# Optimization experiments

Hardware: AMD Instinct MI355X
Metric: run time of the kernel (lower is better)

Reference implementation:

```python
import jax, jax.numpy as jnp
import numpy as np
from jax import lax

T, H, I, E = 1024, 2048, 1024, 16
G, TOPK_GROUP, TOP_K = 4, 2, 4
ROUTED_SCALE = 2.5
W_SCALE = 0.02  # keep activations in a sane range


def setup_inputs() -> dict:
    key = jax.random.key(0)
    ks = jax.random.split(key, 7)
    return {
        "hidden_states": jax.random.normal(ks[0], (T, H), jnp.float32),
        "gate_w": jax.random.normal(ks[1], (E, H), jnp.float32) * W_SCALE,
        "e_bias": jax.random.normal(ks[2], (E,), jnp.float32),
        "w_gate_up": jax.random.normal(ks[3], (E, 2 * I, H), jnp.float32) * W_SCALE,
        "w_down": jax.random.normal(ks[4], (E, H, I), jnp.float32) * W_SCALE,
        "shared_w_gate_up": jax.random.normal(ks[5], (2 * I, H), jnp.float32) * W_SCALE,
        "shared_w_down": jax.random.normal(ks[6], (H, I), jnp.float32) * W_SCALE,
    }


def _grouped_topk(scores, e_bias):
    # scores: sigmoid router scores [T, E]
    scores_b = scores + e_bias[None, :]
    # group score = sum of top-2 biased scores within each group (bias branch)
    group_scores = jnp.sum(lax.top_k(scores_b.reshape(-1, G, E // G), 2)[0], axis=-1)  # [T, G]
    _, group_idx = lax.top_k(group_scores, TOPK_GROUP)  # [T, topk_group]
    group_mask = jnp.any(jax.nn.one_hot(group_idx, G, dtype=jnp.bool_), axis=1)  # [T, G]
    score_mask = jnp.repeat(group_mask, E // G, axis=-1)  # [T, E]
    tmp = jnp.where(score_mask, scores_b, 0.0)
    _, topk_ids = lax.top_k(tmp, TOP_K)  # [T, K]
    topk_w = jnp.take_along_axis(scores, topk_ids, axis=1)  # weights from UNbiased scores
    topk_w = topk_w / jnp.sum(topk_w, axis=-1, keepdims=True)  # renormalize
    return topk_w, topk_ids


def _silu_and_mul(gu):
    g, u = jnp.split(gu, 2, axis=-1)
    return jax.nn.silu(g) * u


def reference(hidden_states, gate_w, e_bias, w_gate_up, w_down,
              shared_w_gate_up, shared_w_down):
    x = hidden_states  # [T, H]
    # shared expert MLP
    shared = _silu_and_mul(x @ shared_w_gate_up.T) @ shared_w_down.T  # [T, H]
    # router
    logits = x @ gate_w.T                      # [T, E]
    scores = jax.nn.sigmoid(logits)
    topk_w, topk_ids = _grouped_topk(scores, e_bias)
    # dense combine weights [T, E] (zero for unselected experts)
    combine = jnp.zeros((T, E), x.dtype).at[jnp.arange(T)[:, None], topk_ids].add(topk_w)
    # routed experts: SwiGLU per expert, combined with routing weights
    gu = jnp.einsum('th,eih->tei', x, w_gate_up)        # [T, E, 2I]
    a = _silu_and_mul(gu)                               # [T, E, I]
    routed = jnp.einsum('tei,ehi,te->th', a, w_down, combine)  # [T, H]
    return routed * ROUTED_SCALE + shared
```

## Files before the change

kernel.cpp:

```cpp
#include <hip/hip_runtime.h>
#include <math.h>

typedef __bf16 bf16;
typedef bf16 bf16x4 __attribute__((ext_vector_type(4)));
typedef bf16 bf16x8 __attribute__((ext_vector_type(8)));
typedef float f32x4 __attribute__((ext_vector_type(4)));

#define T_TOK   1024
#define H_DIM   2048
#define I_DIM   1024
#define E_NUM   16
#define NPAIR_R 4096
#define NPAIR   5120

typedef __attribute__((address_space(3))) unsigned int lds_uint;
typedef __attribute__((address_space(1))) const unsigned int gbl_uint;
__device__ __forceinline__ void gld16(const void* g, void* l) {
  __builtin_amdgcn_global_load_lds((gbl_uint*)g, (lds_uint*)l, 16, 0, 0);
}

__global__ __launch_bounds__(256) void router_kernel(
    const float* __restrict__ x, const float* __restrict__ gate_w,
    const float* __restrict__ e_bias, bf16* __restrict__ xb,
    int* __restrict__ topk_ids, float* __restrict__ topk_w,
    int* __restrict__ counts)
{
  int t = blockIdx.x;
  int tid = threadIdx.x;
  float acc[16];
#pragma unroll
  for (int e = 0; e < 16; ++e) acc[e] = 0.f;
  const float* xr = x + (size_t)t * H_DIM;
  bf16* xbr = xb + (size_t)t * H_DIM;
  for (int h = tid; h < H_DIM; h += 256) {
    float xv = xr[h];
    xbr[h] = (bf16)xv;
#pragma unroll
    for (int e = 0; e < 16; ++e) acc[e] += xv * gate_w[e * H_DIM + h];
  }
#pragma unroll
  for (int e = 0; e < 16; ++e) {
#pragma unroll
    for (int off = 32; off >= 1; off >>= 1)
      acc[e] += __shfl_down(acc[e], off, 64);
  }
  __shared__ float red[4][16];
  int lane = tid & 63, wave = tid >> 6;
  if (lane == 0) {
#pragma unroll
    for (int e = 0; e < 16; ++e) red[wave][e] = acc[e];
  }
  __syncthreads();
  if (tid == 0) {
    float scores[16], sb[16];
    for (int e = 0; e < 16; ++e) {
      float l = red[0][e] + red[1][e] + red[2][e] + red[3][e];
      float s = 1.f / (1.f + expf(-l));
      scores[e] = s;
      sb[e] = s + e_bias[e];
    }
    float gs[4];
    for (int g = 0; g < 4; ++g) {
      float b1 = -1e30f, b2 = -1e30f;
      for (int j = 0; j < 4; ++j) {
        float v = sb[g * 4 + j];
        if (v > b1) { b2 = b1; b1 = v; }
        else if (v > b2) b2 = v;
      }
      gs[g] = b1 + b2;
    }
    int g1 = 0; float bv = gs[0];
    for (int g = 1; g < 4; ++g) if (gs[g] > bv) { bv = gs[g]; g1 = g; }
    int g2 = -1; float bv2 = -1e30f;
    for (int g = 0; g < 4; ++g) if (g != g1 && gs[g] > bv2) { bv2 = gs[g]; g2 = g; }
    float tmp[16];
    for (int e = 0; e < 16; ++e) {
      int grp = e >> 2;
      tmp[e] = (grp == g1 || grp == g2) ? sb[e] : 0.0f;
    }
    bool used[16] = {false};
    int ids[4]; float wv[4]; float wsum = 0.f;
    for (int k = 0; k < 4; ++k) {
      int bi = 0; float bvv = -1e30f;
      for (int i = 0; i < 16; ++i)
        if (!used[i] && tmp[i] > bvv) { bvv = tmp[i]; bi = i; }
      used[bi] = true;
      ids[k] = bi; wv[k] = scores[bi]; wsum += scores[bi];
    }
    float inv = 1.f / wsum;
    for (int k = 0; k < 4; ++k) {
      topk_ids[t * 4 + k] = ids[k];
      topk_w[t * 4 + k] = wv[k] * inv;
      atomicAdd(&counts[ids[k]], 1);
    }
  }
}

__global__ void offsets_kernel(const int* __restrict__ counts, int* __restrict__ off)
{
  if (threadIdx.x == 0 && blockIdx.x == 0) {
    int s = 0;
    for (int e = 0; e < 16; ++e) { off[e] = s; s += counts[e]; }
    off[16] = s;
  }
}

__global__ __launch_bounds__(256) void scatter_kernel(
    const int* __restrict__ topk_ids, const float* __restrict__ topk_w,
    const int* __restrict__ off, int* __restrict__ cursor,
    int* __restrict__ pair_token, float* __restrict__ pair_scale)
{
  int i = blockIdx.x * 256 + threadIdx.x;
  if (i < NPAIR_R) {
    int e = topk_ids[i];
    float w = topk_w[i];
    int pos = atomicAdd(&cursor[e], 1);
    int idx = off[e] + pos;
    pair_token[idx] = i >> 2;
    pair_scale[idx] = 2.5f * w;
  } else if (i < NPAIR) {
    pair_token[i] = i - NPAIR_R;
    pair_scale[i] = 1.0f;
  }
}

__global__ __launch_bounds__(256, 3) void gateup_kernel(
    const bf16* __restrict__ xb, const float* __restrict__ w_gu,
    const float* __restrict__ s_wgu,
    const int* __restrict__ off, const int* __restrict__ pair_token,
    bf16* __restrict__ a_buf)
{
  const int nt = blockIdx.x;
  const int mt = blockIdx.y;
  const int e  = blockIdx.z;
  const int poff = (e < 16) ? off[e]     : NPAIR_R;
  const int pend = (e < 16) ? off[e + 1] : NPAIR;
  const int cnt  = pend - poff;
  if (mt * 128 >= cnt) return;
  const float* __restrict__ B = (e < 16) ? (w_gu + (size_t)e * 2 * I_DIM * H_DIM) : s_wgu;

  __shared__ __align__(16) bf16  As[2][128 * 32];
  __shared__ __align__(16) float Bs[2][128 * 32];

  const int tid = threadIdx.x;
  const int lane = tid & 63;
  const int wave = tid >> 6;
  const int wm = wave >> 1, wn = wave & 1;
  const int c0 = lane >> 4;
  const int fr = lane & 15;

  const bf16* aptr[2];
#pragma unroll
  for (int s = 0; s < 2; ++s) {
    int idx = s * 256 + tid;
    int ar = idx >> 2, ach = idx & 3;
    int sch = ach ^ ((ar >> 1) & 3);
    int p = poff + mt * 128 + ar;
    aptr[s] = xb + (size_t)pair_token[p] * H_DIM + sch * 8;
  }
  const float* bptr[4];
#pragma unroll
  for (int s = 0; s < 4; ++s) {
    int idx = s * 256 + tid;
    int br = idx >> 3, bch = idx & 7;
    int sch = bch ^ (br & 7);
    int rg = nt * 64 + br + (br >= 64 ? 960 : 0);
    bptr[s] = B + (size_t)rg * H_DIM + sch * 4;
  }
  int a_off[4];
#pragma unroll
  for (int mi = 0; mi < 4; ++mi) {
    int ar = wm * 64 + mi * 16 + fr;
    a_off[mi] = ar * 64 + ((c0 ^ ((ar >> 1) & 3)) << 4);
  }
  int b_off[4];
#pragma unroll
  for (int ni = 0; ni < 4; ++ni) {
    int br = wn * 32 + (ni & 1) * 16 + fr + (ni >> 1) * 64;
    b_off[ni] = br * 128 + (((2 * c0) ^ (br & 7)) << 4);
  }

  f32x4 acc[4][4];
  f32x4 zz = {0.f, 0.f, 0.f, 0.f};
#pragma unroll
  for (int mi = 0; mi < 4; ++mi)
#pragma unroll
    for (int ni = 0; ni < 4; ++ni) acc[mi][ni] = zz;

  const int ldso = tid * 16;
#pragma unroll
  for (int s = 0; s < 2; ++s)
    gld16(aptr[s], (char*)(&As[0][0]) + s * 4096 + ldso);
#pragma unroll
  for (int s = 0; s < 4; ++s)
    gld16(bptr[s], (char*)(&Bs[0][0]) + s * 4096 + ldso);
  __syncthreads();

  int cur = 0;
  const int NT = H_DIM / 32;
  for (int t = 0; t < NT; ++t) {
    if (t + 1 < NT) {
      const int k0 = (t + 1) * 32;
#pragma unroll
      for (int s = 0; s < 2; ++s)
        gld16(aptr[s] + k0, (char*)(&As[cur ^ 1][0]) + s * 4096 + ldso);
#pragma unroll
      for (int s = 0; s < 4; ++s)
        gld16(bptr[s] + k0, (char*)(&Bs[cur ^ 1][0]) + s * 4096 + ldso);
    }
    const char* Ab = (const char*)(&As[cur][0]);
    const char* Bb = (const char*)(&Bs[cur][0]);
    bf16x8 af[4], bv[4];
#pragma unroll
    for (int mi = 0; mi < 4; ++mi)
      af[mi] = *(const bf16x8*)(Ab + a_off[mi]);
#pragma unroll
    for (int ni = 0; ni < 4; ++ni) {
      f32x4 x0 = *(const f32x4*)(Bb + b_off[ni]);
      f32x4 x1 = *(const f32x4*)(Bb + (b_off[ni] ^ 16));
      bf16x8 b;
      b[0] = (bf16)x0[0]; b[1] = (bf16)x0[1]; b[2] = (bf16)x0[2]; b[3] = (bf16)x0[3];
      b[4] = (bf16)x1[0]; b[5] = (bf16)x1[1]; b[6] = (bf16)x1[2]; b[7] = (bf16)x1[3];
      bv[ni] = b;
    }
#pragma unroll
    for (int mi = 0; mi < 4; ++mi)
#pragma unroll
      for (int ni = 0; ni < 4; ++ni)
        acc[mi][ni] = __builtin_amdgcn_mfma_f32_16x16x32_bf16(af[mi], bv[ni], acc[mi][ni], 0, 0, 0);
    __syncthreads();
    cur ^= 1;
  }

#pragma unroll
  for (int mi = 0; mi < 4; ++mi) {
#pragma unroll
    for (int reg = 0; reg < 4; ++reg) {
      int r = wm * 64 + mi * 16 + c0 * 4 + reg;
      int rl = mt * 128 + r;
      if (rl < cnt) {
        size_t p = (size_t)(poff + rl);
        bf16* orow = a_buf + p * I_DIM + nt * 64 + wn * 32 + fr;
#pragma unroll
        for (int ni = 0; ni < 2; ++ni) {
          float g = acc[mi][ni][reg];
          float u = acc[mi][ni + 2][reg];
          float sg = g / (1.f + expf(-g));
          orow[ni * 16] = (bf16)(sg * u);
        }
      }
    }
  }
}

__global__ __launch_bounds__(256, 3) void down_kernel(
    const bf16* __restrict__ a_buf, const float* __restrict__ w_dn,
    const float* __restrict__ s_wdn,
    const int* __restrict__ off, const int* __restrict__ pair_token,
    const float* __restrict__ pair_scale, float* __restrict__ out)
{
  const int nt = blockIdx.x;
  const int mt = blockIdx.y;
  const int e  = blockIdx.z;
  const int poff = (e < 16) ? off[e]     : NPAIR_R;
  const int pend = (e < 16) ? off[e + 1] : NPAIR;
  const int cnt  = pend - poff;
  if (mt * 128 >= cnt) return;
  const float* __restrict__ B = (e < 16) ? (w_dn + (size_t)e * H_DIM * I_DIM) : s_wdn;

  __shared__ __align__(16) bf16  As[2][128 * 32];
  __shared__ __align__(16) float Bs[2][128 * 32];

  const int tid = threadIdx.x;
  const int lane = tid & 63;
  const int wave = tid >> 6;
  const int wm = wave >> 1, wn = wave & 1;
  const int c0 = lane >> 4;
  const int fr = lane & 15;

  const bf16* aptr[2];
#pragma unroll
  for (int s = 0; s < 2; ++s) {
    int idx = s * 256 + tid;
    int ar = idx >> 2, ach = idx & 3;
    int sch = ach ^ ((ar >> 1) & 3);
    int p = poff + mt * 128 + ar;
    aptr[s] = a_buf + (size_t)p * I_DIM + sch * 8;
  }
  const float* bptr[4];
#pragma unroll
  for (int s = 0; s < 4; ++s) {
    int idx = s * 256 + tid;
    int br = idx >> 3, bch = idx & 7;
    int sch = bch ^ (br & 7);
    bptr[s] = B + (size_t)(nt * 128 + br) * I_DIM + sch * 4;
  }
  int a_off[4];
#pragma unroll
  for (int mi = 0; mi < 4; ++mi) {
    int ar = wm * 64 + mi * 16 + fr;
    a_off[mi] = ar * 64 + ((c0 ^ ((ar >> 1) & 3)) << 4);
  }
  int b_off[4];
#pragma unroll
  for (int ni = 0; ni < 4; ++ni) {
    int br = wn * 64 + ni * 16 + fr;
    b_off[ni] = br * 128 + (((2 * c0) ^ (br & 7)) << 4);
  }

  f32x4 acc[4][4];
  f32x4 zz = {0.f, 0.f, 0.f, 0.f};
#pragma unroll
  for (int mi = 0; mi < 4; ++mi)
#pragma unroll
    for (int ni = 0; ni < 4; ++ni) acc[mi][ni] = zz;

  const int ldso = tid * 16;
#pragma unroll
  for (int s = 0; s < 2; ++s)
    gld16(aptr[s], (char*)(&As[0][0]) + s * 4096 + ldso);
#pragma unroll
  for (int s = 0; s < 4; ++s)
    gld16(bptr[s], (char*)(&Bs[0][0]) + s * 4096 + ldso);
  __syncthreads();

  int cur = 0;
  const int NT = I_DIM / 32;
  for (int t = 0; t < NT; ++t) {
    if (t + 1 < NT) {
      const int k0 = (t + 1) * 32;
#pragma unroll
      for (int s = 0; s < 2; ++s)
        gld16(aptr[s] + k0, (char*)(&As[cur ^ 1][0]) + s * 4096 + ldso);
#pragma unroll
      for (int s = 0; s < 4; ++s)
        gld16(bptr[s] + k0, (char*)(&Bs[cur ^ 1][0]) + s * 4096 + ldso);
    }
    const char* Ab = (const char*)(&As[cur][0]);
    const char* Bb = (const char*)(&Bs[cur][0]);
    bf16x8 af[4], bv[4];
#pragma unroll
    for (int mi = 0; mi < 4; ++mi)
      af[mi] = *(const bf16x8*)(Ab + a_off[mi]);
#pragma unroll
    for (int ni = 0; ni < 4; ++ni) {
      f32x4 x0 = *(const f32x4*)(Bb + b_off[ni]);
      f32x4 x1 = *(const f32x4*)(Bb + (b_off[ni] ^ 16));
      bf16x8 b;
      b[0] = (bf16)x0[0]; b[1] = (bf16)x0[1]; b[2] = (bf16)x0[2]; b[3] = (bf16)x0[3];
      b[4] = (bf16)x1[0]; b[5] = (bf16)x1[1]; b[6] = (bf16)x1[2]; b[7] = (bf16)x1[3];
      bv[ni] = b;
    }
#pragma unroll
    for (int mi = 0; mi < 4; ++mi)
#pragma unroll
      for (int ni = 0; ni < 4; ++ni)
        acc[mi][ni] = __builtin_amdgcn_mfma_f32_16x16x32_bf16(af[mi], bv[ni], acc[mi][ni], 0, 0, 0);
    __syncthreads();
    cur ^= 1;
  }

  const int colb = nt * 128 + wn * 64;
#pragma unroll
  for (int mi = 0; mi < 4; ++mi) {
#pragma unroll
    for (int reg = 0; reg < 4; ++reg) {
      int r = wm * 64 + mi * 16 + c0 * 4 + reg;
      int rl = mt * 128 + r;
      if (rl < cnt) {
        int p = poff + rl;
        int tok = pair_token[p];
        float sc = pair_scale[p];
        float* orow = out + (size_t)tok * H_DIM + colb + fr;
#pragma unroll
        for (int ni = 0; ni < 4; ++ni)
          atomicAdd(&orow[ni * 16], acc[mi][ni][reg] * sc);
      }
    }
  }
}

extern "C" void kernel_launch(void* const* d_in, const int* in_sizes, int n_in,
                              void* d_out, int out_size, void* d_ws, size_t ws_size,
                              hipStream_t stream)
{
  const float* x     = (const float*)d_in[0];
  const float* gatew = (const float*)d_in[1];
  const float* ebias = (const float*)d_in[2];
  const float* w_gu  = (const float*)d_in[3];
  const float* w_dn  = (const float*)d_in[4];
  const float* s_wgu = (const float*)d_in[5];
  const float* s_wdn = (const float*)d_in[6];
  float* out = (float*)d_out;

  char* ws = (char*)d_ws;
  int*   off        = (int*)(ws + 0);
  int*   counts     = (int*)(ws + 128);
  int*   cursor     = (int*)(ws + 192);
  int*   topk_ids   = (int*)(ws + 256);
  float* topk_w     = (float*)(ws + 16640);
  int*   pair_token = (int*)(ws + 33024);
  float* pair_scale = (float*)(ws + 53504);
  bf16*  x_bf16     = (bf16*)(ws + 73984);
  bf16*  a_buf      = (bf16*)(ws + 73984 + 4194304);

  hipMemsetAsync(out, 0, (size_t)T_TOK * H_DIM * sizeof(float), stream);
  hipMemsetAsync(ws + 128, 0, 128, stream);

  router_kernel<<<T_TOK, 256, 0, stream>>>(x, gatew, ebias, x_bf16, topk_ids, topk_w, counts);
  offsets_kernel<<<1, 64, 0, stream>>>(counts, off);
  scatter_kernel<<<NPAIR / 256, 256, 0, stream>>>(topk_ids, topk_w, off, cursor,
                                                  pair_token, pair_scale);
  dim3 g1(16, 8, 17);
  gateup_kernel<<<g1, 256, 0, stream>>>(x_bf16, w_gu, s_wgu, off, pair_token, a_buf);
  dim3 g2(16, 8, 17);
  down_kernel<<<g2, 256, 0, stream>>>(a_buf, w_dn, s_wdn, off, pair_token, pair_scale, out);
}
```

Before: 646.2 us.

## Triple-buffer GEMM loads, fuse output zeroing into router, merge pair-building kernels

The gate-up and down GEMMs move from double to triple buffering of LDS tiles, using explicit vmcnt waits and raw barriers so two stages of global-to-LDS loads stay in flight, and launch bounds drop from 3 to 2 blocks per SIMD to fit the larger LDS. The output memset moves into the router kernel, which now zeroes each output row. The offsets and scatter kernels merge into one single-block kernel that uses shared-memory atomics. Together these aim to hide load latency and cut launch overhead, at the cost of lower occupancy and a serial single-block pair build.

```diff
diff --git a/kernel.cpp b/kernel.cpp
--- a/kernel.cpp
+++ b/kernel.cpp
@@ -22,6 +22,7 @@
 __global__ __launch_bounds__(256) void router_kernel(
     const float* __restrict__ x, const float* __restrict__ gate_w,
     const float* __restrict__ e_bias, bf16* __restrict__ xb,
+    float* __restrict__ out,
     int* __restrict__ topk_ids, float* __restrict__ topk_w,
     int* __restrict__ counts)
 {
@@ -32,9 +33,11 @@
   for (int e = 0; e < 16; ++e) acc[e] = 0.f;
   const float* xr = x + (size_t)t * H_DIM;
   bf16* xbr = xb + (size_t)t * H_DIM;
+  float* outr = out + (size_t)t * H_DIM;
   for (int h = tid; h < H_DIM; h += 256) {
     float xv = xr[h];
     xbr[h] = (bf16)xv;
+    outr[h] = 0.f;
 #pragma unroll
     for (int e = 0; e < 16; ++e) acc[e] += xv * gate_w[e * H_DIM + h];
   }
@@ -96,35 +99,36 @@
   }
 }
 
-__global__ void offsets_kernel(const int* __restrict__ counts, int* __restrict__ off)
-{
-  if (threadIdx.x == 0 && blockIdx.x == 0) {
-    int s = 0;
-    for (int e = 0; e < 16; ++e) { off[e] = s; s += counts[e]; }
-    off[16] = s;
-  }
-}
-
-__global__ __launch_bounds__(256) void scatter_kernel(
+__global__ __launch_bounds__(1024) void build_pairs_kernel(
     const int* __restrict__ topk_ids, const float* __restrict__ topk_w,
-    const int* __restrict__ off, int* __restrict__ cursor,
+    const int* __restrict__ counts, int* __restrict__ off,
     int* __restrict__ pair_token, float* __restrict__ pair_scale)
 {
-  int i = blockIdx.x * 256 + threadIdx.x;
-  if (i < NPAIR_R) {
-    int e = topk_ids[i];
-    float w = topk_w[i];
-    int pos = atomicAdd(&cursor[e], 1);
-    int idx = off[e] + pos;
-    pair_token[idx] = i >> 2;
-    pair_scale[idx] = 2.5f * w;
-  } else if (i < NPAIR) {
-    pair_token[i] = i - NPAIR_R;
-    pair_scale[i] = 1.0f;
-  }
-}
-
-__global__ __launch_bounds__(256, 3) void gateup_kernel(
+  __shared__ int s_off[17];
+  __shared__ int s_cur[16];
+  int tid = threadIdx.x;
+  if (tid == 0) {
+    int s = 0;
+    for (int e = 0; e < 16; ++e) { s_off[e] = s; off[e] = s; s += counts[e]; }
+    s_off[16] = s; off[16] = s;
+  }
+  if (tid < 16) s_cur[tid] = 0;
+  __syncthreads();
+  for (int i = tid; i < NPAIR; i += 1024) {
+    if (i < NPAIR_R) {
+      int e = topk_ids[i];
+      int pos = atomicAdd(&s_cur[e], 1);
+      int idx = s_off[e] + pos;
+      pair_token[idx] = i >> 2;
+      pair_scale[idx] = 2.5f * topk_w[i];
+    } else {
+      pair_token[i] = i - NPAIR_R;
+      pair_scale[i] = 1.0f;
+    }
+  }
+}
+
+__global__ __launch_bounds__(256, 2) void gateup_kernel(
     const bf16* __restrict__ xb, const float* __restrict__ w_gu,
     const float* __restrict__ s_wgu,
     const int* __restrict__ off, const int* __restrict__ pair_token,
@@ -139,8 +143,8 @@
   if (mt * 128 >= cnt) return;
   const float* __restrict__ B = (e < 16) ? (w_gu + (size_t)e * 2 * I_DIM * H_DIM) : s_wgu;
 
-  __shared__ __align__(16) bf16  As[2][128 * 32];
-  __shared__ __align__(16) float Bs[2][128 * 32];
+  __shared__ __align__(16) bf16  As[3 * 4096];
+  __shared__ __align__(16) float Bs[3 * 4096];
 
   const int tid = threadIdx.x;
   const int lane = tid & 63;
@@ -188,28 +192,17 @@
     for (int ni = 0; ni < 4; ++ni) acc[mi][ni] = zz;
 
   const int ldso = tid * 16;
-#pragma unroll
-  for (int s = 0; s < 2; ++s)
-    gld16(aptr[s], (char*)(&As[0][0]) + s * 4096 + ldso);
-#pragma unroll
-  for (int s = 0; s < 4; ++s)
-    gld16(bptr[s], (char*)(&Bs[0][0]) + s * 4096 + ldso);
-  __syncthreads();
-
-  int cur = 0;
-  const int NT = H_DIM / 32;
-  for (int t = 0; t < NT; ++t) {
-    if (t + 1 < NT) {
-      const int k0 = (t + 1) * 32;
-#pragma unroll
-      for (int s = 0; s < 2; ++s)
-        gld16(aptr[s] + k0, (char*)(&As[cur ^ 1][0]) + s * 4096 + ldso);
-#pragma unroll
-      for (int s = 0; s < 4; ++s)
-        gld16(bptr[s] + k0, (char*)(&Bs[cur ^ 1][0]) + s * 4096 + ldso);
-    }
-    const char* Ab = (const char*)(&As[cur][0]);
-    const char* Bb = (const char*)(&Bs[cur][0]);
+  auto stage = [&](int k0, int b) {
+#pragma unroll
+    for (int s = 0; s < 2; ++s)
+      gld16(aptr[s] + k0, (char*)As + b * 8192 + s * 4096 + ldso);
+#pragma unroll
+    for (int s = 0; s < 4; ++s)
+      gld16(bptr[s] + k0, (char*)Bs + b * 16384 + s * 4096 + ldso);
+  };
+  auto compute = [&](int b) {
+    const char* Ab = (const char*)As + b * 8192;
+    const char* Bb = (const char*)Bs + b * 16384;
     bf16x8 af[4], bv[4];
 #pragma unroll
     for (int mi = 0; mi < 4; ++mi)
@@ -218,19 +211,37 @@
     for (int ni = 0; ni < 4; ++ni) {
       f32x4 x0 = *(const f32x4*)(Bb + b_off[ni]);
       f32x4 x1 = *(const f32x4*)(Bb + (b_off[ni] ^ 16));
-      bf16x8 b;
-      b[0] = (bf16)x0[0]; b[1] = (bf16)x0[1]; b[2] = (bf16)x0[2]; b[3] = (bf16)x0[3];
-      b[4] = (bf16)x1[0]; b[5] = (bf16)x1[1]; b[6] = (bf16)x1[2]; b[7] = (bf16)x1[3];
-      bv[ni] = b;
+      bf16x8 t;
+      t[0] = (bf16)x0[0]; t[1] = (bf16)x0[1]; t[2] = (bf16)x0[2]; t[3] = (bf16)x0[3];
+      t[4] = (bf16)x1[0]; t[5] = (bf16)x1[1]; t[6] = (bf16)x1[2]; t[7] = (bf16)x1[3];
+      bv[ni] = t;
     }
 #pragma unroll
     for (int mi = 0; mi < 4; ++mi)
 #pragma unroll
       for (int ni = 0; ni < 4; ++ni)
         acc[mi][ni] = __builtin_amdgcn_mfma_f32_16x16x32_bf16(af[mi], bv[ni], acc[mi][ni], 0, 0, 0);
-    __syncthreads();
-    cur ^= 1;
-  }
+  };
+
+  const int NT = H_DIM / 32;
+  stage(0, 0);
+  stage(32, 1);
+  int ca = 0, cb = 1, cc = 2;
+  for (int t = 0; t + 2 < NT; ++t) {
+    stage((t + 2) * 32, cc);
+    asm volatile("s_waitcnt vmcnt(12)" ::: "memory");
+    __builtin_amdgcn_s_barrier();
+    compute(ca);
+    asm volatile("" ::: "memory");
+    __builtin_amdgcn_s_barrier();
+    int tmp = ca; ca = cb; cb = cc; cc = tmp;
+  }
+  asm volatile("s_waitcnt vmcnt(6)" ::: "memory");
+  __builtin_amdgcn_s_barrier();
+  compute(ca);
+  asm volatile("s_waitcnt vmcnt(0)" ::: "memory");
+  __builtin_amdgcn_s_barrier();
+  compute(cb);
 
 #pragma unroll
   for (int mi = 0; mi < 4; ++mi) {
@@ -253,7 +264,7 @@
   }
 }
 
-__global__ __launch_bounds__(256, 3) void down_kernel(
+__global__ __launch_bounds__(256, 2) void down_kernel(
     const bf16* __restrict__ a_buf, const float* __restrict__ w_dn,
     const float* __restrict__ s_wdn,
     const int* __restrict__ off, const int* __restrict__ pair_token,
@@ -268,8 +279,8 @@
   if (mt * 128 >= cnt) return;
   const float* __restrict__ B = (e < 16) ? (w_dn + (size_t)e * H_DIM * I_DIM) : s_wdn;
 
-  __shared__ __align__(16) bf16  As[2][128 * 32];
-  __shared__ __align__(16) float Bs[2][128 * 32];
+  __shared__ __align__(16) bf16  As[3 * 4096];
+  __shared__ __align__(16) float Bs[3 * 4096];
 
   const int tid = threadIdx.x;
   const int lane = tid & 63;
@@ -316,28 +327,17 @@
     for (int ni = 0; ni < 4; ++ni) acc[mi][ni] = zz;
 
   const int ldso = tid * 16;
-#pragma unroll
-  for (int s = 0; s < 2; ++s)
-    gld16(aptr[s], (char*)(&As[0][0]) + s * 4096 + ldso);
-#pragma unroll
-  for (int s = 0; s < 4; ++s)
-    gld16(bptr[s], (char*)(&Bs[0][0]) + s * 4096 + ldso);
-  __syncthreads();
-
-  int cur = 0;
-  const int NT = I_DIM / 32;
-  for (int t = 0; t < NT; ++t) {
-    if (t + 1 < NT) {
-      const int k0 = (t + 1) * 32;
-#pragma unroll
-      for (int s = 0; s < 2; ++s)
-        gld16(aptr[s] + k0, (char*)(&As[cur ^ 1][0]) + s * 4096 + ldso);
-#pragma unroll
-      for (int s = 0; s < 4; ++s)
-        gld16(bptr[s] + k0, (char*)(&Bs[cur ^ 1][0]) + s * 4096 + ldso);
-    }
-    const char* Ab = (const char*)(&As[cur][0]);
-    const char* Bb = (const char*)(&Bs[cur][0]);
+  auto stage = [&](int k0, int b) {
+#pragma unroll
+    for (int s = 0; s < 2; ++s)
+      gld16(aptr[s] + k0, (char*)As + b * 8192 + s * 4096 + ldso);
+#pragma unroll
+    for (int s = 0; s < 4; ++s)
+      gld16(bptr[s] + k0, (char*)Bs + b * 16384 + s * 4096 + ldso);
+  };
+  auto compute = [&](int b) {
+    const char* Ab = (const char*)As + b * 8192;
+    const char* Bb = (const char*)Bs + b * 16384;
     bf16x8 af[4], bv[4];
 #pragma unroll
     for (int mi = 0; mi < 4; ++mi)
@@ -346,19 +346,37 @@
     for (int ni = 0; ni < 4; ++ni) {
       f32x4 x0 = *(const f32x4*)(Bb + b_off[ni]);
       f32x4 x1 = *(const f32x4*)(Bb + (b_off[ni] ^ 16));
-      bf16x8 b;
-      b[0] = (bf16)x0[0]; b[1] = (bf16)x0[1]; b[2] = (bf16)x0[2]; b[3] = (bf16)x0[3];
-      b[4] = (bf16)x1[0]; b[5] = (bf16)x1[1]; b[6] = (bf16)x1[2]; b[7] = (bf16)x1[3];
-      bv[ni] = b;
+      bf16x8 t;
+      t[0] = (bf16)x0[0]; t[1] = (bf16)x0[1]; t[2] = (bf16)x0[2]; t[3] = (bf16)x0[3];
+      t[4] = (bf16)x1[0]; t[5] = (bf16)x1[1]; t[6] = (bf16)x1[2]; t[7] = (bf16)x1[3];
+      bv[ni] = t;
     }
 #pragma unroll
     for (int mi = 0; mi < 4; ++mi)
 #pragma unroll
       for (int ni = 0; ni < 4; ++ni)
         acc[mi][ni] = __builtin_amdgcn_mfma_f32_16x16x32_bf16(af[mi], bv[ni], acc[mi][ni], 0, 0, 0);
-    __syncthreads();
-    cur ^= 1;
-  }
+  };
+
+  const int NT = I_DIM / 32;
+  stage(0, 0);
+  stage(32, 1);
+  int ca = 0, cb = 1, cc = 2;
+  for (int t = 0; t + 2 < NT; ++t) {
+    stage((t + 2) * 32, cc);
+    asm volatile("s_waitcnt vmcnt(12)" ::: "memory");
+    __builtin_amdgcn_s_barrier();
+    compute(ca);
+    asm volatile("" ::: "memory");
+    __builtin_amdgcn_s_barrier();
+    int tmp = ca; ca = cb; cb = cc; cc = tmp;
+  }
+  asm volatile("s_waitcnt vmcnt(6)" ::: "memory");
+  __builtin_amdgcn_s_barrier();
+  compute(ca);
+  asm volatile("s_waitcnt vmcnt(0)" ::: "memory");
+  __builtin_amdgcn_s_barrier();
+  compute(cb);
 
   const int colb = nt * 128 + wn * 64;
 #pragma unroll
@@ -396,7 +414,6 @@
   char* ws = (char*)d_ws;
   int*   off        = (int*)(ws + 0);
   int*   counts     = (int*)(ws + 128);
-  int*   cursor     = (int*)(ws + 192);
   int*   topk_ids   = (int*)(ws + 256);
   float* topk_w     = (float*)(ws + 16640);
   int*   pair_token = (int*)(ws + 33024);
@@ -404,13 +421,12 @@
   bf16*  x_bf16     = (bf16*)(ws + 73984);
   bf16*  a_buf      = (bf16*)(ws + 73984 + 4194304);
 
-  hipMemsetAsync(out, 0, (size_t)T_TOK * H_DIM * sizeof(float), stream);
-  hipMemsetAsync(ws + 128, 0, 128, stream);
-
-  router_kernel<<<T_TOK, 256, 0, stream>>>(x, gatew, ebias, x_bf16, topk_ids, topk_w, counts);
-  offsets_kernel<<<1, 64, 0, stream>>>(counts, off);
-  scatter_kernel<<<NPAIR / 256, 256, 0, stream>>>(topk_ids, topk_w, off, cursor,
-                                                  pair_token, pair_scale);
+  hipMemsetAsync(ws + 128, 0, 64, stream);
+
+  router_kernel<<<T_TOK, 256, 0, stream>>>(x, gatew, ebias, x_bf16, out,
+                                           topk_ids, topk_w, counts);
+  build_pairs_kernel<<<1, 1024, 0, stream>>>(topk_ids, topk_w, counts, off,
+                                             pair_token, pair_scale);
   dim3 g1(16, 8, 17);
   gateup_kernel<<<g1, 256, 0, stream>>>(x_bf16, w_gu, s_wgu, off, pair_token, a_buf);
   dim3 g2(16, 8, 17);
```

New measurement: 666.4 us. 3.1% more time.
